# Performance work log

Hardware: AMD Instinct MI355X
Metric: run time of the kernel (lower is better)

## Reference

```python
import jax, jax.numpy as jnp
import numpy as np

EPS = 1e-7        # min norm to avoid div-by-zero
BALL_EPS = 1e-5   # Poincare-ball boundary clip


def _norm(x):
    return jnp.maximum(jnp.linalg.norm(x, axis=-1, keepdims=True), EPS)


def expmap0(u, c):
    sc = jnp.sqrt(c)
    n = _norm(u)
    return jnp.tanh(sc * n) * u / (sc * n)


def logmap0(p, c):
    sc = jnp.sqrt(c)
    n = _norm(p)
    return jnp.arctanh(jnp.minimum(sc * n, 1.0 - BALL_EPS)) * p / (sc * n)


def proj(x, c):
    # project onto the ball of radius (1-eps)/sqrt(c)
    n = _norm(x)
    maxn = (1.0 - BALL_EPS) / jnp.sqrt(c)
    return jnp.where(n > maxn, x * (maxn / n), x)


def mobius_matvec(W, x, c):
    # Mobius matrix-vector multiply on the Poincare ball
    sc = jnp.sqrt(c)
    xn = _norm(x)                       # [N,1]
    mx = x @ W                          # [N,D]
    mxn = _norm(mx)
    t = jnp.tanh((mxn / xn) * jnp.arctanh(jnp.minimum(sc * xn, 1.0 - BALL_EPS)))
    return t * mx / (sc * mxn)


def spmm(rows, cols, vals, x):
    # sparse(adj) @ x, adjacency in COO form
    return jax.ops.segment_sum(vals[:, None] * x[cols], rows, num_segments=x.shape[0])


def hgc_layer(x, rows, cols, vals, W, c, c_lin):
    t = logmap0(x, c)                               # to tangent space at origin
    h = proj(mobius_matvec(W, t, c_lin), c_lin)     # LinearHyperbolic (c=1.0, no activation)
    s = spmm(rows, cols, vals, h)                   # HyperbolicAggregation: adj @ h
    agg = proj(expmap0(s, c), c)
    a = jax.nn.relu(logmap0(agg, c))                # ActivationHyperbolic (relu, c_in=c_out=c)
    return proj(expmap0(a, c), c)


def setup_inputs() -> dict:
    key = jax.random.key(0)
    ks = jax.random.split(key, 7)
    N, D, E = 10000, 1433, 100000
    x = jax.random.normal(ks[0], (N, D), jnp.float32) * 0.1  # keep points off the boundary
    rows = jax.random.randint(ks[1], (E,), 0, N)
    cols = jax.random.randint(ks[2], (E,), 0, N)
    vals = jax.random.uniform(ks[3], (E,), jnp.float32) / 10.0  # ~normalized adjacency weights
    scale = 1.0 / np.sqrt(D)
    W0 = jax.random.normal(ks[4], (D, D), jnp.float32) * scale
    W1 = jax.random.normal(ks[5], (D, D), jnp.float32) * scale
    W2 = jax.random.normal(ks[6], (D, D), jnp.float32) * scale
    return {"x": x, "W0": W0, "W1": W1, "W2": W2, "vals": vals, "rows": rows, "cols": cols}


def reference(x, W0, W1, W2, vals, rows, cols):
    c = jnp.float32(0.4)       # c_map == c0 for every layer in the source
    c_lin = jnp.float32(1.0)   # LinearHyperbolic hard-coded c
    h = expmap0(x, c)
    for W in (W0, W1, W2):
        h = hgc_layer(h, rows, cols, vals, W, c, c_lin)
    return h
```

## Files before the change

### kernel.cpp

```cpp
#include <hip/hip_runtime.h>

typedef unsigned short u16;
typedef unsigned int   u32;

#define M_ROWS 10000
#define D_DIM  1433
#define KPAD   1536
#define MPAD   10240
#define N_EDGE 100000
#define HPAD   1440
#define HP32   720
#define NKT    24
#define EPS    1e-7f
#define BEPS   1e-5f
#define SC     0.6324555320336759f

typedef __bf16 bf16x8 __attribute__((ext_vector_type(8)));
typedef float  f32x4  __attribute__((ext_vector_type(4)));
typedef u32    u32x4  __attribute__((ext_vector_type(4)));

__device__ __forceinline__ u16 f2bf(float f) {
  union { float f; unsigned u; } v; v.f = f;
  unsigned r = v.u + 0x7FFFu + ((v.u >> 16) & 1u);
  return (u16)(r >> 16);
}
__device__ __forceinline__ u32 pack2bf(float lo, float hi) {
  return (u32)f2bf(lo) | ((u32)f2bf(hi) << 16);
}
__device__ __forceinline__ float bflo(u32 u) { return __uint_as_float(u << 16); }
__device__ __forceinline__ float bfhi(u32 u) { return __uint_as_float(u & 0xFFFF0000u); }

__device__ __forceinline__ float atanh_f(float y) {
  return 0.5f * logf((1.f + y) / (1.f - y));
}

__device__ __forceinline__ void gl_lds16(const u16* g, u16* l) {
  __builtin_amdgcn_global_load_lds((const __attribute__((address_space(1))) void*)(const void*)g,
                                   (__attribute__((address_space(3))) void*)(void*)l,
                                   16, 0, 0);
}

__global__ __launch_bounds__(512, 1) void gemm256(
    const u16* __restrict__ A,
    const u16* __restrict__ B,
    u16* __restrict__ C,
    float* __restrict__ nrm)
{
  __shared__ u16 lds[2][2][256 * 64];

  const int tid  = threadIdx.x;
  const int lane = tid & 63;
  const int w    = tid >> 6;
  const int wr   = w >> 2;
  const int wc   = w & 3;

  const int flat = blockIdx.x;
  const int wgid = (flat & 7) * 30 + (flat >> 3);
  const int gy = wgid % 6;
  const int gx = wgid / 6;
  const long arow0 = (long)gx * 256;
  const long brow0 = (long)gy * 256;

  f32x4 acc[8][4] = {};

  const int sr8 = lane >> 3;
  const int scb = ((lane & 7) << 4) ^ (sr8 << 4);

  auto STG_B = [&](int b, int kt) {
    const long k0 = (long)kt * 64 + (scb >> 1);
#pragma unroll
    for (int l = 0; l < 4; ++l) {
      const int r   = l * 64 + w * 8 + sr8;
      const int dst = l * 4096 + w * 512;
      gl_lds16(B + (brow0 + r) * KPAD + k0, &lds[b][1][dst]);
    }
  };
  auto STG_A = [&](int b, int kt, int sel) {
    const long k0 = (long)kt * 64 + (scb >> 1);
#pragma unroll
    for (int li = 0; li < 2; ++li) {
      const int l   = sel + 2 * li;
      const int r   = l * 64 + w * 8 + sr8;
      const int dst = l * 4096 + w * 512;
      gl_lds16(A + (arow0 + r) * KPAD + k0, &lds[b][0][dst]);
    }
  };

  STG_B(0, 0); STG_A(0, 0, 0); STG_A(0, 0, 1);
  asm volatile("s_waitcnt vmcnt(0)" ::: "memory");
  __builtin_amdgcn_s_barrier();

  for (int kt = 0; kt < NKT; ++kt) {
    const int b = kt & 1;
    const bool pf = (kt + 1 < NKT);

    bf16x8 b0[4], b1[4], a0[4], a1[4];
#pragma unroll
    for (int ni = 0; ni < 4; ++ni) {
      const int row = wc * 64 + ni * 16 + (lane & 15);
      const int kb0 = (((lane >> 4) << 4)) ^ ((row & 7) << 4);
      const int kb1 = (64 + ((lane >> 4) << 4)) ^ ((row & 7) << 4);
      b0[ni] = *(const bf16x8*)&lds[b][1][row * 64 + (kb0 >> 1)];
      b1[ni] = *(const bf16x8*)&lds[b][1][row * 64 + (kb1 >> 1)];
    }
#pragma unroll
    for (int ml = 0; ml < 4; ++ml) {
      const int row = wr * 128 + ml * 16 + (lane & 15);
      const int kb0 = (((lane >> 4) << 4)) ^ ((row & 7) << 4);
      const int kb1 = (64 + ((lane >> 4) << 4)) ^ ((row & 7) << 4);
      a0[ml] = *(const bf16x8*)&lds[b][0][row * 64 + (kb0 >> 1)];
      a1[ml] = *(const bf16x8*)&lds[b][0][row * 64 + (kb1 >> 1)];
    }
    if (pf) { STG_B(b ^ 1, kt + 1); STG_A(b ^ 1, kt + 1, 0); }
    __builtin_amdgcn_s_setprio(1);
#pragma unroll
    for (int ml = 0; ml < 4; ++ml)
#pragma unroll
      for (int ni = 0; ni < 4; ++ni)
        acc[ml][ni] = __builtin_amdgcn_mfma_f32_16x16x32_bf16(a0[ml], b0[ni], acc[ml][ni], 0, 0, 0);
#pragma unroll
    for (int ml = 0; ml < 4; ++ml)
#pragma unroll
      for (int ni = 0; ni < 4; ++ni)
        acc[ml][ni] = __builtin_amdgcn_mfma_f32_16x16x32_bf16(a1[ml], b1[ni], acc[ml][ni], 0, 0, 0);
    __builtin_amdgcn_s_setprio(0);
    if (pf) asm volatile("s_waitcnt vmcnt(6)" ::: "memory");
    else    asm volatile("s_waitcnt vmcnt(0)" ::: "memory");
    __builtin_amdgcn_s_barrier();

    bf16x8 c0[4], c1[4];
#pragma unroll
    for (int ml = 0; ml < 4; ++ml) {
      const int row = wr * 128 + (4 + ml) * 16 + (lane & 15);
      const int kb0 = (((lane >> 4) << 4)) ^ ((row & 7) << 4);
      const int kb1 = (64 + ((lane >> 4) << 4)) ^ ((row & 7) << 4);
      c0[ml] = *(const bf16x8*)&lds[b][0][row * 64 + (kb0 >> 1)];
      c1[ml] = *(const bf16x8*)&lds[b][0][row * 64 + (kb1 >> 1)];
    }
    if (pf) STG_A(b ^ 1, kt + 1, 1);
    __builtin_amdgcn_s_setprio(1);
#pragma unroll
    for (int ml = 0; ml < 4; ++ml)
#pragma unroll
      for (int ni = 0; ni < 4; ++ni)
        acc[4 + ml][ni] = __builtin_amdgcn_mfma_f32_16x16x32_bf16(c0[ml], b0[ni], acc[4 + ml][ni], 0, 0, 0);
#pragma unroll
    for (int ml = 0; ml < 4; ++ml)
#pragma unroll
      for (int ni = 0; ni < 4; ++ni)
        acc[4 + ml][ni] = __builtin_amdgcn_mfma_f32_16x16x32_bf16(c1[ml], b1[ni], acc[4 + ml][ni], 0, 0, 0);
    __builtin_amdgcn_s_setprio(0);
    if (pf) asm volatile("s_waitcnt vmcnt(2)" ::: "memory");
    __builtin_amdgcn_s_barrier();
  }

  const int orw = (lane >> 4) * 4;
  const int ocl = lane & 15;

#pragma unroll
  for (int mi = 0; mi < 8; ++mi)
#pragma unroll
    for (int r = 0; r < 4; ++r) {
      float s = 0.f;
#pragma unroll
      for (int ni = 0; ni < 4; ++ni) {
        const long j = brow0 + wc * 64 + ni * 16 + ocl;
        const float v = acc[mi][ni][r];
        s += (j < D_DIM) ? v * v : 0.f;
      }
      s += __shfl_xor(s, 1, 64);
      s += __shfl_xor(s, 2, 64);
      s += __shfl_xor(s, 4, 64);
      s += __shfl_xor(s, 8, 64);
      if ((lane & 15) == 0)
        atomicAdd(&nrm[arow0 + wr * 128 + mi * 16 + orw + r], s);
    }

#pragma unroll
  for (int mi = 0; mi < 8; ++mi) {
    const long i0 = arow0 + wr * 128 + mi * 16 + orw;
    if (i0 >= M_ROWS) continue;
#pragma unroll
    for (int ni = 0; ni < 4; ++ni) {
      const long j = brow0 + wc * 64 + ni * 16 + ocl;
      if (j >= HPAD) continue;
#pragma unroll
      for (int r = 0; r < 4; ++r) {
        const long i = i0 + r;
        if (i < M_ROWS) C[i * HPAD + j] = (j < D_DIM) ? f2bf(acc[mi][ni][r]) : (u16)0;
      }
    }
  }
}

__device__ __forceinline__ float2 block_reduce2(float a, float b) {
  __shared__ float sa[4], sb[4];
#pragma unroll
  for (int off = 32; off > 0; off >>= 1) {
    a += __shfl_down(a, off, 64);
    b += __shfl_down(b, off, 64);
  }
  const int tid = threadIdx.x;
  if ((tid & 63) == 0) { sa[tid >> 6] = a; sb[tid >> 6] = b; }
  __syncthreads();
  const float ra = sa[0] + sa[1] + sa[2] + sa[3];
  const float rb = sb[0] + sb[1] + sb[2] + sb[3];
  __syncthreads();
  return make_float2(ra, rb);
}

__global__ __launch_bounds__(256) void pre_k(const float* __restrict__ x,
                                             u16* __restrict__ t,
                                             float* __restrict__ xn) {
  const long i = blockIdx.x;
  const int tid = threadIdx.x;
  u16* trow = t + i * KPAD;
  if (i >= M_ROWS) {
#pragma unroll
    for (int jj = 0; jj < 6; ++jj) { int j = tid + jj * 256; if (j < KPAD) trow[j] = 0; }
    return;
  }
  const float* xr = x + i * D_DIM;
  float v[6]; float s2 = 0.f;
#pragma unroll
  for (int jj = 0; jj < 6; ++jj) {
    int j = tid + jj * 256;
    v[jj] = (j < D_DIM) ? xr[j] : 0.f;
    s2 += v[jj] * v[jj];
  }
  s2 = block_reduce2(s2, 0.f).x;
  const float nx_t = sqrtf(s2);
  const float nx   = fmaxf(nx_t, EPS);
  const float al   = tanhf(SC * nx) / (SC * nx);
  const float n1   = fmaxf(al * nx_t, EPS);
  const float be   = atanh_f(fminf(SC * n1, 1.f - BEPS)) / (SC * n1);
  const float sca  = al * be;
  if (tid == 0) xn[i] = fmaxf(sca * nx_t, EPS);
#pragma unroll
  for (int jj = 0; jj < 6; ++jj) {
    int j = tid + jj * 256;
    if (j < KPAD) trow[j] = (j < D_DIM) ? f2bf(sca * v[jj]) : (u16)0;
  }
}

__global__ void zero_f(float* p, int n) {
  int i = blockIdx.x * 256 + threadIdx.x;
  if (i < n) p[i] = 0.f;
}

__global__ void fold_k(const int* __restrict__ ecol, const float* __restrict__ eval,
                       const float* __restrict__ nrm, const float* __restrict__ xn,
                       u32* __restrict__ pe, int E) {
  const int e = blockIdx.x * 256 + threadIdx.x;
  if (e >= E) return;
  const int c = ecol[e];
  const float realn = sqrtf(nrm[c]);
  const float mxn   = fmaxf(realn, EPS);
  const float xi    = xn[c];
  const float tf    = tanhf((mxn / xi) * atanh_f(fminf(xi, 1.f - BEPS)));
  float S = tf / mxn;
  const float hn = fmaxf(S * realn, EPS);
  const float maxn = 1.f - BEPS;
  if (hn > maxn) S *= maxn / hn;
  pe[e] = ((u32)c << 16) | (u32)f2bf(eval[e] * S);
}

__global__ __launch_bounds__(256) void spmm_post(const int* __restrict__ rp,
                                                 const u32* __restrict__ pe,
                                                 const u32* __restrict__ mxp,
                                                 u16* __restrict__ t,
                                                 float* __restrict__ xn,
                                                 float* __restrict__ out,
                                                 const int last) {
  const long r = blockIdx.x;
  const int tid = threadIdx.x;
  if (r >= M_ROWS) {
    if (!last && tid < 192) {
      u32* trow32 = (u32*)(t + r * KPAD);
#pragma unroll
      for (int k = 0; k < 4; ++k) trow32[4 * tid + k] = 0u;
    }
    return;
  }
  const bool act = tid < 180;
  const long boff = 4 * tid;
  float a[8] = {0.f, 0.f, 0.f, 0.f, 0.f, 0.f, 0.f, 0.f};
  const int e0 = rp[r], e1 = rp[r + 1];
  int e = e0;
  for (; e + 7 < e1; e += 8) {
    u32 pp[8];
#pragma unroll
    for (int j = 0; j < 8; ++j) pp[j] = pe[e + j];
    if (act) {
      u32x4 q[8];
#pragma unroll
      for (int j = 0; j < 8; ++j)
        q[j] = *(const u32x4*)&mxp[(long)(pp[j] >> 16) * HP32 + boff];
#pragma unroll
      for (int j = 0; j < 8; ++j) {
        const float w = bflo(pp[j]);
#pragma unroll
        for (int k = 0; k < 4; ++k) {
          a[2 * k]     += w * bflo(q[j][k]);
          a[2 * k + 1] += w * bfhi(q[j][k]);
        }
      }
    }
  }
  for (; e + 3 < e1; e += 4) {
    u32 pp[4];
#pragma unroll
    for (int j = 0; j < 4; ++j) pp[j] = pe[e + j];
    if (act) {
      u32x4 q[4];
#pragma unroll
      for (int j = 0; j < 4; ++j)
        q[j] = *(const u32x4*)&mxp[(long)(pp[j] >> 16) * HP32 + boff];
#pragma unroll
      for (int j = 0; j < 4; ++j) {
        const float w = bflo(pp[j]);
#pragma unroll
        for (int k = 0; k < 4; ++k) {
          a[2 * k]     += w * bflo(q[j][k]);
          a[2 * k + 1] += w * bfhi(q[j][k]);
        }
      }
    }
  }
  for (; e < e1; ++e) {
    const u32 p0 = pe[e];
    if (act) {
      const u32x4 q0 = *(const u32x4*)&mxp[(long)(p0 >> 16) * HP32 + boff];
      const float w0 = bflo(p0);
#pragma unroll
      for (int k = 0; k < 4; ++k) {
        a[2 * k]     += w0 * bflo(q0[k]);
        a[2 * k + 1] += w0 * bfhi(q0[k]);
      }
    }
  }
  float s2 = 0.f, s2p = 0.f;
#pragma unroll
  for (int k = 0; k < 8; ++k) {
    const int col = 8 * tid + k;
    const float v = (act && col < D_DIM) ? a[k] : 0.f;
    a[k] = v;
    s2 += v * v;
    const float p = fmaxf(v, 0.f);
    s2p += p * p;
  }
  const float2 red = block_reduce2(s2, s2p);
  const float ns_t  = sqrtf(red.x);
  const float nsp_t = sqrtf(red.y);
  const float maxn = (1.f - BEPS) / SC;
  const float ns = fmaxf(ns_t, EPS);
  const float al = tanhf(SC * ns) / (SC * ns);
  const float n1 = fmaxf(al * ns_t, EPS);
  const float be = (n1 > maxn) ? (maxn / n1) : 1.f;
  const float n2 = fmaxf(be * al * ns_t, EPS);
  const float lam = atanh_f(fminf(SC * n2, 1.f - BEPS)) / (SC * n2);
  const float g = lam * be * al;
  const float na_t = g * nsp_t;
  const float n3 = fmaxf(na_t, EPS);
  const float mu = tanhf(SC * n3) / (SC * n3);
  const float n4 = fmaxf(mu * na_t, EPS);
  const float nu = (n4 > maxn) ? (maxn / n4) : 1.f;
  const float T = nu * mu * g;
  if (last) {
    if (act) {
      float* orow = out + r * (long)D_DIM;
#pragma unroll
      for (int k = 0; k < 8; ++k) {
        const int col = 8 * tid + k;
        if (col < D_DIM) orow[col] = T * fmaxf(a[k], 0.f);
      }
    }
  } else {
    const float nh_t = T * nsp_t;
    const float n5 = fmaxf(nh_t, EPS);
    const float kap = atanh_f(fminf(SC * n5, 1.f - BEPS)) / (SC * n5);
    const float F = kap * T;
    if (tid == 0) xn[r] = fmaxf(F * nsp_t, EPS);
    u32* trow32 = (u32*)(t + r * KPAD);
    if (act) {
#pragma unroll
      for (int k = 0; k < 4; ++k)
        trow32[4 * tid + k] = pack2bf(F * fmaxf(a[2 * k], 0.f), F * fmaxf(a[2 * k + 1], 0.f));
    } else if (tid < 192) {
#pragma unroll
      for (int k = 0; k < 4; ++k) trow32[4 * tid + k] = 0u;
    }
  }
}

__global__ void wt_conv(const float* __restrict__ W, u16* __restrict__ Wt) {
  __shared__ float tile[32][33];
  const int kb = blockIdx.x * 32, nb = blockIdx.y * 32;
  const int tx = threadIdx.x, ty = threadIdx.y;
#pragma unroll
  for (int r = 0; r < 32; r += 8) {
    const int k = kb + ty + r, n = nb + tx;
    tile[ty + r][tx] = (k < D_DIM && n < D_DIM) ? W[(long)k * D_DIM + n] : 0.f;
  }
  __syncthreads();
#pragma unroll
  for (int r = 0; r < 32; r += 8) {
    const int n = nb + ty + r, k = kb + tx;
    if (n < KPAD && k < KPAD) Wt[(long)n * KPAD + k] = f2bf(tile[tx][ty + r]);
  }
}

__global__ void zero_int(int* p, int n) {
  int i = blockIdx.x * 256 + threadIdx.x;
  if (i < n) p[i] = 0;
}
__global__ void hist_k(const int* __restrict__ rows, int* __restrict__ counts, int E) {
  int e = blockIdx.x * 256 + threadIdx.x;
  if (e < E) atomicAdd(&counts[rows[e]], 1);
}
__global__ __launch_bounds__(1024) void scan_rp(const int* __restrict__ counts,
                                                int* __restrict__ rp, int n) {
  __shared__ int sd[1024];
  __shared__ int carry_s;
  const int tid = threadIdx.x;
  if (tid == 0) { carry_s = 0; rp[0] = 0; }
  __syncthreads();
  for (int base = 0; base < n; base += 1024) {
    const int i = base + tid;
    sd[tid] = (i < n) ? counts[i] : 0;
    __syncthreads();
    for (int off = 1; off < 1024; off <<= 1) {
      const int tv = (tid >= off) ? sd[tid - off] : 0;
      __syncthreads();
      sd[tid] += tv;
      __syncthreads();
    }
    const int carry = carry_s;
    if (i < n) rp[i + 1] = carry + sd[tid];
    __syncthreads();
    if (tid == 1023) carry_s = carry + sd[1023];
    __syncthreads();
  }
}
__global__ void scatter_k(const int* __restrict__ rows, const int* __restrict__ cols,
                          const float* __restrict__ vals, const int* __restrict__ rp,
                          int* __restrict__ cursor, int* __restrict__ ecol,
                          float* __restrict__ eval, int E) {
  int e = blockIdx.x * 256 + threadIdx.x;
  if (e < E) {
    const int r = rows[e];
    const int pos = rp[r] + atomicAdd(&cursor[r], 1);
    ecol[pos] = cols[e];
    eval[pos] = vals[e];
  }
}

extern "C" void kernel_launch(void* const* d_in, const int* in_sizes, int n_in,
                              void* d_out, int out_size, void* d_ws, size_t ws_size,
                              hipStream_t stream) {
  (void)in_sizes; (void)n_in; (void)out_size; (void)ws_size;
  const float* x    = (const float*)d_in[0];
  const float* W[3] = {(const float*)d_in[1], (const float*)d_in[2], (const float*)d_in[3]};
  const float* vals = (const float*)d_in[4];
  const int*   rows = (const int*)d_in[5];
  const int*   cols = (const int*)d_in[6];
  float* out = (float*)d_out;

  char* base = (char*)d_ws;
  size_t off = 0;
  auto take = [&](size_t bytes) {
    void* q = base + off;
    off = (off + bytes + 255) & ~(size_t)255;
    return q;
  };
  u16*   t    = (u16*)take((size_t)MPAD * KPAD * 2);
  u16*   Wt   = (u16*)take((size_t)KPAD * KPAD * 2);
  u16*   mx   = (u16*)take((size_t)M_ROWS * HPAD * 2);
  float* nrm3 = (float*)take((size_t)3 * MPAD * 4);
  float* xn   = (float*)take((size_t)M_ROWS * 4);
  int*   cnt  = (int*)take((size_t)M_ROWS * 2 * 4);
  int*   rp   = (int*)take((size_t)(M_ROWS + 1) * 4);
  int*   ecol = (int*)take((size_t)N_EDGE * 4);
  float* eval = (float*)take((size_t)N_EDGE * 4);
  u32*   pe   = (u32*)take((size_t)N_EDGE * 4);

  zero_int<<<(2 * M_ROWS + 255) / 256, 256, 0, stream>>>(cnt, 2 * M_ROWS);
  hist_k<<<(N_EDGE + 255) / 256, 256, 0, stream>>>(rows, cnt, N_EDGE);
  scan_rp<<<1, 1024, 0, stream>>>(cnt, rp, M_ROWS);
  scatter_k<<<(N_EDGE + 255) / 256, 256, 0, stream>>>(rows, cols, vals, rp,
                                                      cnt + M_ROWS, ecol, eval, N_EDGE);
  zero_f<<<(3 * MPAD + 255) / 256, 256, 0, stream>>>(nrm3, 3 * MPAD);

  pre_k<<<MPAD, 256, 0, stream>>>(x, t, xn);

  for (int L = 0; L < 3; ++L) {
    float* nrm = nrm3 + (size_t)L * MPAD;
    wt_conv<<<dim3(48, 48), dim3(32, 8), 0, stream>>>(W[L], Wt);
    gemm256<<<240, 512, 0, stream>>>(t, Wt, mx, nrm);
    fold_k<<<(N_EDGE + 255) / 256, 256, 0, stream>>>(ecol, eval, nrm, xn, pe, N_EDGE);
    spmm_post<<<MPAD, 256, 0, stream>>>(rp, pe, (const u32*)mx, t, xn, out, (L == 2) ? 1 : 0);
  }
}
```

Before: 370.1 us.

## Trim GEMM K padding to 1472 and unify SpMM gather loop with 12-edge batches

```diff
diff --git a/kernel.cpp b/kernel.cpp
--- a/kernel.cpp
+++ b/kernel.cpp
@@ -5,12 +5,13 @@
 
 #define M_ROWS 10000
 #define D_DIM  1433
-#define KPAD   1536
+#define KPAD   1472
+#define NPAD   1536
 #define MPAD   10240
 #define N_EDGE 100000
 #define HPAD   1440
 #define HP32   720
-#define NKT    24
+#define NKT    23
 #define EPS    1e-7f
 #define BEPS   1e-5f
 #define SC     0.6324555320336759f
@@ -275,7 +276,7 @@
   const long r = blockIdx.x;
   const int tid = threadIdx.x;
   if (r >= M_ROWS) {
-    if (!last && tid < 192) {
+    if (!last && tid < 184) {
       u32* trow32 = (u32*)(t + r * KPAD);
 #pragma unroll
       for (int k = 0; k < 4; ++k) trow32[4 * tid + k] = 0u;
@@ -286,56 +287,27 @@
   const long boff = 4 * tid;
   float a[8] = {0.f, 0.f, 0.f, 0.f, 0.f, 0.f, 0.f, 0.f};
   const int e0 = rp[r], e1 = rp[r + 1];
-  int e = e0;
-  for (; e + 7 < e1; e += 8) {
-    u32 pp[8];
-#pragma unroll
-    for (int j = 0; j < 8; ++j) pp[j] = pe[e + j];
+  for (int e = e0; e < e1; e += 12) {
+    u32 pp[12]; float w[12];
+#pragma unroll
+    for (int j = 0; j < 12; ++j) {
+      const int ee = e + j;
+      const int ec = (ee < e1) ? ee : (e1 - 1);
+      pp[j] = pe[ec];
+      w[j]  = (ee < e1) ? bflo(pp[j]) : 0.f;
+    }
     if (act) {
-      u32x4 q[8];
-#pragma unroll
-      for (int j = 0; j < 8; ++j)
+      u32x4 q[12];
+#pragma unroll
+      for (int j = 0; j < 12; ++j)
         q[j] = *(const u32x4*)&mxp[(long)(pp[j] >> 16) * HP32 + boff];
 #pragma unroll
-      for (int j = 0; j < 8; ++j) {
-        const float w = bflo(pp[j]);
+      for (int j = 0; j < 12; ++j) {
 #pragma unroll
         for (int k = 0; k < 4; ++k) {
-          a[2 * k]     += w * bflo(q[j][k]);
-          a[2 * k + 1] += w * bfhi(q[j][k]);
+          a[2 * k]     += w[j] * bflo(q[j][k]);
+          a[2 * k + 1] += w[j] * bfhi(q[j][k]);
         }
-      }
-    }
-  }
-  for (; e + 3 < e1; e += 4) {
-    u32 pp[4];
-#pragma unroll
-    for (int j = 0; j < 4; ++j) pp[j] = pe[e + j];
-    if (act) {
-      u32x4 q[4];
-#pragma unroll
-      for (int j = 0; j < 4; ++j)
-        q[j] = *(const u32x4*)&mxp[(long)(pp[j] >> 16) * HP32 + boff];
-#pragma unroll
-      for (int j = 0; j < 4; ++j) {
-        const float w = bflo(pp[j]);
-#pragma unroll
-        for (int k = 0; k < 4; ++k) {
-          a[2 * k]     += w * bflo(q[j][k]);
-          a[2 * k + 1] += w * bfhi(q[j][k]);
-        }
-      }
-    }
-  }
-  for (; e < e1; ++e) {
-    const u32 p0 = pe[e];
-    if (act) {
-      const u32x4 q0 = *(const u32x4*)&mxp[(long)(p0 >> 16) * HP32 + boff];
-      const float w0 = bflo(p0);
-#pragma unroll
-      for (int k = 0; k < 4; ++k) {
-        a[2 * k]     += w0 * bflo(q0[k]);
-        a[2 * k + 1] += w0 * bfhi(q0[k]);
       }
     }
   }
@@ -386,7 +358,7 @@
 #pragma unroll
       for (int k = 0; k < 4; ++k)
         trow32[4 * tid + k] = pack2bf(F * fmaxf(a[2 * k], 0.f), F * fmaxf(a[2 * k + 1], 0.f));
-    } else if (tid < 192) {
+    } else if (tid < 184) {
 #pragma unroll
       for (int k = 0; k < 4; ++k) trow32[4 * tid + k] = 0u;
     }
@@ -406,7 +378,7 @@
 #pragma unroll
   for (int r = 0; r < 32; r += 8) {
     const int n = nb + ty + r, k = kb + tx;
-    if (n < KPAD && k < KPAD) Wt[(long)n * KPAD + k] = f2bf(tile[tx][ty + r]);
+    if (n < NPAD && k < KPAD) Wt[(long)n * KPAD + k] = f2bf(tile[tx][ty + r]);
   }
 }
 
@@ -474,7 +446,7 @@
     return q;
   };
   u16*   t    = (u16*)take((size_t)MPAD * KPAD * 2);
-  u16*   Wt   = (u16*)take((size_t)KPAD * KPAD * 2);
+  u16*   Wt   = (u16*)take((size_t)NPAD * KPAD * 2);
   u16*   mx   = (u16*)take((size_t)M_ROWS * HPAD * 2);
   float* nrm3 = (float*)take((size_t)3 * MPAD * 4);
   float* xn   = (float*)take((size_t)M_ROWS * 4);
@@ -495,7 +467,7 @@
 
   for (int L = 0; L < 3; ++L) {
     float* nrm = nrm3 + (size_t)L * MPAD;
-    wt_conv<<<dim3(48, 48), dim3(32, 8), 0, stream>>>(W[L], Wt);
+    wt_conv<<<dim3(46, 48), dim3(32, 8), 0, stream>>>(W[L], Wt);
     gemm256<<<240, 512, 0, stream>>>(t, Wt, mx, nrm);
     fold_k<<<(N_EDGE + 255) / 256, 256, 0, stream>>>(ecol, eval, nrm, xn, pe, N_EDGE);
     spmm_post<<<MPAD, 256, 0, stream>>>(rp, pe, (const u32*)mx, t, xn, out, (L == 2) ? 1 : 0);
```

Result: no change. 369.5 us (-0.2%).
